# Kernel optimization log

Measured on AMD Instinct MI355X. Metric: run time of the kernel, lower is better.

Reference implementation:

```python
import jax, jax.numpy as jnp
import numpy as np
from jax import lax

# pywt db4 decomposition filters (hardcoded to avoid pywt dependency)
DB4_DEC_LO = np.array([-0.010597401784997278, 0.032883011666982945,
                       0.030841381835986965, -0.18703481171888114,
                       -0.02798376941698385, 0.6308807679295904,
                       0.7148465705525415, 0.23037781330885523], dtype=np.float32)
DB4_DEC_HI = np.array([-0.23037781330885523, 0.7148465705525415,
                       -0.6308807679295904, -0.02798376941698385,
                       0.18703481171888114, 0.030841381835986965,
                       -0.032883011666982945, -0.010597401784997278], dtype=np.float32)

B, T, C = 32, 16384, 64

def setup_inputs() -> dict:
    key = jax.random.key(0)
    x = jax.random.normal(key, (B, T, C), dtype=jnp.float32)
    return {"x": x,
            "dec_lo": jnp.asarray(DB4_DEC_LO),
            "dec_hi": jnp.asarray(DB4_DEC_HI)}

def _depthwise_conv1d(xp, filt, channels):
    # xp: [B, L, C]; filt: [K]; depthwise stride-2 valid cross-correlation
    k = jnp.broadcast_to(filt[:, None, None], (filt.shape[0], 1, channels))  # [K,1,C]
    return lax.conv_general_dilated(
        xp, k, window_strides=(2,), padding='VALID',
        dimension_numbers=('NWC', 'WIO', 'NWC'),
        feature_group_count=channels)

def reference(x, dec_lo, dec_hi):
    channels = x.shape[-1]
    filter_length = dec_lo.shape[0]          # 8 for db4
    pad = filter_length - 1                   # 7
    crop = pad // 2                           # 3
    xp = jnp.pad(x, ((0, 0), (pad, pad), (0, 0)), mode='reflect')
    approx = _depthwise_conv1d(xp, dec_lo, channels)[:, crop:-crop, :]
    detail = _depthwise_conv1d(xp, dec_hi, channels)[:, crop:-crop, :]
    # original concatenates all approx channels then all detail channels
    return jnp.concatenate([approx, detail], axis=-1)  # [B, T/2-2, 2C]
```

## Files before the change

kernel.cpp:

```cpp
#include <hip/hip_runtime.h>


#define BT   32
#define TT   16384
#define CC   64
#define T2   8190
#define OC   128
#define QPT  4
#define NQ   ((T2 + QPT - 1) / QPT)

typedef float vf4 __attribute__((ext_vector_type(4)));

__global__ __launch_bounds__(256) void dwt_db4_quad_kernel(
    const float* __restrict__ x,
    const float* __restrict__ dec_lo,
    const float* __restrict__ dec_hi,
    float* __restrict__ out)
{
    const int tid  = threadIdx.x;
    const int cg   = tid & 15;
    const int qs   = tid >> 4;
    const int quad = blockIdx.x * 16 + qs;
    const int b    = blockIdx.y;
    if (quad >= NQ) return;

    const int t0 = quad * QPT;
    const int c4 = cg * 4;

    float flo[8], fhi[8];
    #pragma unroll
    for (int k = 0; k < 8; ++k) { flo[k] = dec_lo[k]; fhi[k] = dec_hi[k]; }

    const float* __restrict__ xb = x + (size_t)b * TT * CC;

    const int m0 = 2 * t0 - 1;
    vf4 w[15];
    #pragma unroll
    for (int i = 0; i < 15; ++i) {
        int m  = m0 + i;
        int mm = m < 0 ? -m : m;
        mm     = mm > (TT - 1) ? 2 * (TT - 1) - mm : mm;
        w[i] = *reinterpret_cast<const vf4*>(xb + (size_t)mm * CC + c4);
    }

    vf4 alo[QPT], ahi[QPT];
    #pragma unroll
    for (int j = 0; j < QPT; ++j) {
        alo[j] = (vf4)0.0f;
        ahi[j] = (vf4)0.0f;
    }

    #pragma unroll
    for (int j = 0; j < QPT; ++j) {
        #pragma unroll
        for (int k = 0; k < 8; ++k) {
            const vf4 v = w[2 * j + k];
            alo[j] += flo[k] * v;
            ahi[j] += fhi[k] * v;
        }
    }

    float* __restrict__ ob = out + (size_t)b * T2 * OC + (size_t)t0 * OC;
    #pragma unroll
    for (int j = 0; j < QPT; ++j) {
        if (t0 + j < T2) {
            __builtin_nontemporal_store(alo[j],
                reinterpret_cast<vf4*>(ob + (size_t)j * OC + c4));
            __builtin_nontemporal_store(ahi[j],
                reinterpret_cast<vf4*>(ob + (size_t)j * OC + CC + c4));
        }
    }
}

extern "C" void kernel_launch(void* const* d_in, const int* in_sizes, int n_in,
                              void* d_out, int out_size, void* d_ws, size_t ws_size,
                              hipStream_t stream)
{
    const float* x      = (const float*)d_in[0];
    const float* dec_lo = (const float*)d_in[1];
    const float* dec_hi = (const float*)d_in[2];
    float*       out    = (float*)d_out;

    dim3 block(256);
    dim3 grid((NQ + 15) / 16, BT);

    hipLaunchKernelGGL(dwt_db4_quad_kernel, grid, block, 0, stream,
                       x, dec_lo, dec_hi, out);
}
```

Measured before the change: 230.6 us.

## Stage input tiles in LDS via direct global-to-LDS loads

Each block now owns a tile of 64 output time steps. It copies the 144 reflect-padded input rows that tile needs into shared memory with global_load_lds 16-byte transfers, then each thread reads its 14 overlapping rows from LDS. Before, each thread fetched 15 overlapping rows from global memory and leaned on the cache for reuse. The aim is to cut redundant global traffic and let the hardware move data straight into LDS. The cost is a block-wide barrier and about 36 KB of LDS per block, which limits how many blocks can be resident per CU.

After: 231.9 us. About the same (+0.6%).

```diff
diff --git a/kernel.cpp b/kernel.cpp
--- a/kernel.cpp
+++ b/kernel.cpp
@@ -1,57 +1,72 @@
 #include <hip/hip_runtime.h>
 
 
-#define BT   32
-#define TT   16384
-#define CC   64
-#define T2   8190
-#define OC   128
-#define QPT  4
-#define NQ   ((T2 + QPT - 1) / QPT)
+#define BT    32
+#define TT    16384
+#define CC    64
+#define T2    8190
+#define OC    128
+#define TB    64
+#define NTILE ((T2 + TB - 1) / TB)
+#define SLOTS 2304
 
 typedef float vf4 __attribute__((ext_vector_type(4)));
 
-__global__ __launch_bounds__(256) void dwt_db4_quad_kernel(
+__global__ __launch_bounds__(256, 4) void dwt_db4_lds_kernel(
     const float* __restrict__ x,
     const float* __restrict__ dec_lo,
     const float* __restrict__ dec_hi,
     float* __restrict__ out)
 {
+    __shared__ float lds[SLOTS * 4];
+
     const int tid  = threadIdx.x;
-    const int cg   = tid & 15;
-    const int qs   = tid >> 4;
-    const int quad = blockIdx.x * 16 + qs;
+    const int tile = blockIdx.x;
     const int b    = blockIdx.y;
-    if (quad >= NQ) return;
 
-    const int t0 = quad * QPT;
-    const int c4 = cg * 4;
+    const int t0 = tile * TB;
+    const int m0 = 2 * t0 - 1;
+
+    const float* __restrict__ xb = x + (size_t)b * TT * CC;
 
     float flo[8], fhi[8];
     #pragma unroll
     for (int k = 0; k < 8; ++k) { flo[k] = dec_lo[k]; fhi[k] = dec_hi[k]; }
 
-    const float* __restrict__ xb = x + (size_t)b * TT * CC;
-
-    const int m0 = 2 * t0 - 1;
-    vf4 w[15];
+    const int lane = tid & 63;
+    const int wv   = tid >> 6;
     #pragma unroll
-    for (int i = 0; i < 15; ++i) {
-        int m  = m0 + i;
+    for (int it = 0; it < 9; ++it) {
+        const int base = it * 256 + wv * 64;
+        const int slot = base + lane;
+        const int r    = slot >> 4;
+        const int c4   = (slot & 15) * 4;
+        int m  = m0 + r;
         int mm = m < 0 ? -m : m;
         mm     = mm > (TT - 1) ? 2 * (TT - 1) - mm : mm;
-        w[i] = *reinterpret_cast<const vf4*>(xb + (size_t)mm * CC + c4);
+        const float* gp = xb + (size_t)mm * CC + c4;
+        __builtin_amdgcn_global_load_lds(
+            (const __attribute__((address_space(1))) unsigned int*)gp,
+            (__attribute__((address_space(3))) unsigned int*)&lds[(size_t)base * 4],
+            16, 0, 0);
     }
+    __syncthreads();
 
-    vf4 alo[QPT], ahi[QPT];
+    const int cg = tid & 15;
+    const int ts = tid >> 4;
+    const int c4 = cg * 4;
+
+    vf4 w[14];
     #pragma unroll
-    for (int j = 0; j < QPT; ++j) {
-        alo[j] = (vf4)0.0f;
-        ahi[j] = (vf4)0.0f;
-    }
+    for (int i = 0; i < 14; ++i)
+        w[i] = *reinterpret_cast<const vf4*>(&lds[(size_t)(8 * ts + i) * CC + c4]);
+
+    vf4 alo[4], ahi[4];
+    #pragma unroll
+    for (int j = 0; j < 4; ++j) { alo[j] = (vf4)0.0f; ahi[j] = (vf4)0.0f; }
 
     #pragma unroll
-    for (int j = 0; j < QPT; ++j) {
+    for (int j = 0; j < 4; ++j) {
         #pragma unroll
         for (int k = 0; k < 8; ++k) {
             const vf4 v = w[2 * j + k];
@@ -60,10 +75,11 @@
         }
     }
 
-    float* __restrict__ ob = out + (size_t)b * T2 * OC + (size_t)t0 * OC;
+    const int tbase = t0 + ts * 4;
+    float* __restrict__ ob = out + (size_t)b * T2 * OC + (size_t)tbase * OC;
     #pragma unroll
-    for (int j = 0; j < QPT; ++j) {
-        if (t0 + j < T2) {
+    for (int j = 0; j < 4; ++j) {
+        if (tbase + j < T2) {
             __builtin_nontemporal_store(alo[j],
                 reinterpret_cast<vf4*>(ob + (size_t)j * OC + c4));
             __builtin_nontemporal_store(ahi[j],
@@ -82,8 +98,8 @@
     float*       out    = (float*)d_out;
 
     dim3 block(256);
-    dim3 grid((NQ + 15) / 16, BT);
+    dim3 grid(NTILE, BT);
 
-    hipLaunchKernelGGL(dwt_db4_quad_kernel, grid, block, 0, stream,
+    hipLaunchKernelGGL(dwt_db4_lds_kernel, grid, block, 0, stream,
                        x, dec_lo, dec_hi, out);
 }
```
